# Kernel optimization log

Measured on AMD Instinct MI355X. Metric: run time of the kernel, lower is better.

## Reference

```python
import jax, jax.numpy as jnp
import numpy as np

N_NODES = 100000
N_EDGES = 1600000
IN_CH = 128
EMB = 64


def _init_linear(key, fan_in, fan_out):
    kw, kb = jax.random.split(key)
    scale = 1.0 / np.sqrt(fan_in)
    W = jax.random.uniform(kw, (fan_in, fan_out), jnp.float32, -scale, scale)
    b = jax.random.uniform(kb, (fan_out,), jnp.float32, -scale, scale)
    return W, b


def setup_inputs() -> dict:
    key = jax.random.key(0)
    ks = jax.random.split(key, 6)
    x = jax.random.normal(ks[0], (N_NODES, IN_CH), jnp.float32)
    edge_index = jax.random.randint(ks[1], (2, N_EDGES), 0, N_NODES)
    batch = jnp.zeros((N_NODES,), jnp.int32)
    # conv1 MLP: in_channels -> 32 -> 64 ; conv2 MLP: 64 -> 64 -> embedding_dim
    W1, b1 = _init_linear(ks[2], IN_CH, 32)
    W2, b2 = _init_linear(ks[3], 32, 64)
    W3, b3 = _init_linear(ks[4], 64, 64)
    W4, b4 = _init_linear(ks[5], 64, EMB)
    return {"x": x, "edge_index": edge_index, "batch": batch,
            "W1": W1, "b1": b1, "W2": W2, "b2": b2,
            "W3": W3, "b3": b3, "W4": W4, "b4": b4}


def _mlp(h, Wa, ba, Wb, bb):
    # PyG MLP: Linear -> act -> Linear (plain last layer)
    return jax.nn.relu(h @ Wa + ba) @ Wb + bb


def _gin_conv(x, src, dst, Wa, ba, Wb, bb):
    # out_i = MLP((1+eps)*x_i + sum_{j->i} x_j), eps = 0 (GINConv default)
    agg = jax.ops.segment_sum(x[src], dst, num_segments=N_NODES)  # [N, d]
    return _mlp(x + agg, Wa, ba, Wb, bb)


def reference(x, edge_index, batch, W1, b1, W2, b2, W3, b3, W4, b4):
    src, dst = edge_index[0], edge_index[1]
    h = jax.nn.relu(_gin_conv(x, src, dst, W1, b1, W2, b2))  # [N, 64]
    h = jax.nn.relu(_gin_conv(h, src, dst, W3, b3, W4, b4))  # [N, EMB]
    # batch is overwritten with zeros in the original forward -> single graph
    pooled = jnp.mean(h, axis=0, keepdims=True)  # [1, EMB]
    return h, pooled
```

## Files before the change

### kernel.cpp

```cpp
#include <hip/hip_runtime.h>

#define NN 100000
#define NE 1600000
#define NLB 256
#define CHUNK (NE / NLB)
#define NB 196
#define BN 512

__device__ __forceinline__ float bf2f(unsigned short u) {
    return __uint_as_float(((unsigned int)u) << 16);
}
__device__ __forceinline__ unsigned short f2bf(float f) {
    unsigned int u = __float_as_uint(f);
    return (unsigned short)((u + 0x7FFFu + ((u >> 16) & 1u)) >> 16);
}

__global__ __launch_bounds__(256) void k_front(const int* __restrict__ src,
                                               const int* __restrict__ dst,
                                               int* __restrict__ pairs,
                                               int* __restrict__ tstart,
                                               int* __restrict__ tcnt,
                                               int* __restrict__ btot,
                                               const float* __restrict__ x,
                                               const float* __restrict__ W1,
                                               unsigned short* __restrict__ z1) {
    __shared__ float Ws[128 * 32];
    __shared__ float xs[32][129];
    __shared__ int cnt[NB];
    __shared__ int sc[256];
    __shared__ int cur[NB];
    int tid = threadIdx.x;
    if (blockIdx.x < NLB) {
        int blk = blockIdx.x;
        int e0 = blk * CHUNK;
        for (int i = tid; i < NB; i += 256) cnt[i] = 0;
        __syncthreads();
        for (int i = tid; i < CHUNK; i += 256) atomicAdd(&cnt[dst[e0 + i] >> 9], 1);
        __syncthreads();
        sc[tid] = (tid < NB) ? cnt[tid] : 0;
        __syncthreads();
        for (int off = 1; off < 256; off <<= 1) {
            int v = (tid >= off) ? sc[tid - off] : 0;
            __syncthreads();
            sc[tid] += v;
            __syncthreads();
        }
        if (tid < NB) {
            int excl = sc[tid] - cnt[tid];
            cur[tid] = excl;
            tstart[blk * NB + tid] = excl;
            tcnt[blk * NB + tid]   = cnt[tid];
            atomicAdd(&btot[tid], cnt[tid]);
        }
        __syncthreads();
        for (int i = tid; i < CHUNK; i += 256) {
            int d = dst[e0 + i], s = src[e0 + i];
            int p = atomicAdd(&cur[d >> 9], 1);
            pairs[e0 + p] = ((d & (BN - 1)) << 17) | s;
        }
    } else {
        int bid = blockIdx.x - NLB;
        for (int i = tid; i < 1024; i += 256) {
            float4 w = ((const float4*)W1)[i];
            float* d = &Ws[i * 4];
            d[0] = w.x; d[1] = w.y; d[2] = w.z; d[3] = w.w;
        }
        int n_loc = tid >> 3;
        int j0    = (tid & 7) * 4;
        for (int base = bid * 32; base < NN; base += 1024 * 32) {
            __syncthreads();
            for (int t = tid; t < 1024; t += 256) {
                int n = t >> 5, c = t & 31;
                float4 v = ((const float4*)(x + (size_t)(base + n) * 128))[c];
                float* d = &xs[n][c * 4];
                d[0] = v.x; d[1] = v.y; d[2] = v.z; d[3] = v.w;
            }
            __syncthreads();
            float a0 = 0.f, a1 = 0.f, a2 = 0.f, a3 = 0.f;
            #pragma unroll 8
            for (int k = 0; k < 128; k++) {
                float xv = xs[n_loc][k];
                float4 w = *(const float4*)&Ws[k * 32 + j0];
                a0 = fmaf(xv, w.x, a0); a1 = fmaf(xv, w.y, a1);
                a2 = fmaf(xv, w.z, a2); a3 = fmaf(xv, w.w, a3);
            }
            ushort4 o = { f2bf(a0), f2bf(a1), f2bf(a2), f2bf(a3) };
            *(ushort4*)&z1[(size_t)(base + n_loc) * 32 + j0] = o;
        }
    }
}

__global__ __launch_bounds__(1024) void k_build(const int* __restrict__ pairs,
                                                const int* __restrict__ tstart,
                                                const int* __restrict__ tcnt,
                                                const int* __restrict__ btot,
                                                int* __restrict__ csr,
                                                int* __restrict__ row,
                                                int* __restrict__ rend) {
    __shared__ int segS[NLB], segL[NLB];
    __shared__ int ncnt[BN];
    __shared__ int nbase[BN + 1];
    __shared__ int sc[256];
    __shared__ int sc2[256];
    __shared__ int base_s;
    int tid = threadIdx.x, b = blockIdx.x;

    if (tid < 256) sc2[tid] = (tid < NB) ? btot[tid] : 0;
    __syncthreads();
    for (int off = 1; off < 256; off <<= 1) {
        int v = 0;
        if (tid < 256 && tid >= off) v = sc2[tid - off];
        __syncthreads();
        if (tid < 256) sc2[tid] += v;
        __syncthreads();
    }
    if (tid == 0) base_s = (b == 0) ? 0 : sc2[b - 1];
    if (tid < NLB) {
        segS[tid] = tid * CHUNK + tstart[tid * NB + b];
        segL[tid] = tcnt[tid * NB + b];
    }
    for (int i = tid; i < BN; i += 1024) ncnt[i] = 0;
    __syncthreads();

    int wave = tid >> 6, lane = tid & 63;
    for (int s = wave; s < NLB; s += 16) {
        int st = segS[s], len = segL[s];
        for (int i = lane; i < len; i += 64)
            atomicAdd(&ncnt[pairs[st + i] >> 17], 1);
    }
    __syncthreads();

    int c0 = 0, c1 = 0, tsum = 0;
    if (tid < 256) { c0 = ncnt[2 * tid]; c1 = ncnt[2 * tid + 1]; tsum = c0 + c1; sc[tid] = tsum; }
    __syncthreads();
    for (int off = 1; off < 256; off <<= 1) {
        int v = 0;
        if (tid < 256 && tid >= off) v = sc[tid - off];
        __syncthreads();
        if (tid < 256) sc[tid] += v;
        __syncthreads();
    }
    if (tid < 256) {
        int excl = sc[tid] - tsum;
        nbase[2 * tid]     = excl;
        nbase[2 * tid + 1] = excl + c0;
        if (tid == 255) nbase[BN] = sc[255];
    }
    __syncthreads();

    int base = base_s;
    if (tid < BN) {
        int n = b * BN + tid;
        if (n < NN) { row[n] = base + nbase[tid]; rend[n] = base + nbase[tid + 1]; }
        ncnt[tid] = 0;
    }
    __syncthreads();

    for (int s = wave; s < NLB; s += 16) {
        int st = segS[s], len = segL[s];
        for (int i = lane; i < len; i += 64) {
            int p = pairs[st + i];
            int ln = p >> 17;
            int pos = atomicAdd(&ncnt[ln], 1);
            csr[base + nbase[ln] + pos] = p & 0x1FFFF;
        }
    }
}

__global__ __launch_bounds__(256) void k_gather32(const int* __restrict__ row,
                                                  const int* __restrict__ rend,
                                                  const int* __restrict__ csr,
                                                  const unsigned short* __restrict__ z,
                                                  float* __restrict__ agg) {
    int n = blockIdx.x * 8 + (threadIdx.x >> 5);
    int f = threadIdx.x & 31;
    int j = row[n], e = rend[n];
    float a0 = 0.f, a1 = 0.f, a2 = 0.f, a3 = 0.f;
    for (; j + 3 < e; j += 4) {
        int i0 = csr[j], i1 = csr[j + 1], i2 = csr[j + 2], i3 = csr[j + 3];
        a0 += bf2f(z[(size_t)i0 * 32 + f]);
        a1 += bf2f(z[(size_t)i1 * 32 + f]);
        a2 += bf2f(z[(size_t)i2 * 32 + f]);
        a3 += bf2f(z[(size_t)i3 * 32 + f]);
    }
    for (; j < e; j++) a0 += bf2f(z[(size_t)csr[j] * 32 + f]);
    agg[(size_t)n * 32 + f] = (a0 + a1) + (a2 + a3);
}

__global__ __launch_bounds__(256) void k_gather64(const int* __restrict__ row,
                                                  const int* __restrict__ rend,
                                                  const int* __restrict__ csr,
                                                  const unsigned short* __restrict__ z,
                                                  float* __restrict__ agg) {
    int n = blockIdx.x * 4 + (threadIdx.x >> 6);
    int f = threadIdx.x & 63;
    int j = row[n], e = rend[n];
    float a0 = 0.f, a1 = 0.f, a2 = 0.f, a3 = 0.f;
    for (; j + 7 < e; j += 8) {
        int i0 = csr[j],     i1 = csr[j + 1], i2 = csr[j + 2], i3 = csr[j + 3];
        int i4 = csr[j + 4], i5 = csr[j + 5], i6 = csr[j + 6], i7 = csr[j + 7];
        float v0 = bf2f(z[(size_t)i0 * 64 + f]);
        float v1 = bf2f(z[(size_t)i1 * 64 + f]);
        float v2 = bf2f(z[(size_t)i2 * 64 + f]);
        float v3 = bf2f(z[(size_t)i3 * 64 + f]);
        float v4 = bf2f(z[(size_t)i4 * 64 + f]);
        float v5 = bf2f(z[(size_t)i5 * 64 + f]);
        float v6 = bf2f(z[(size_t)i6 * 64 + f]);
        float v7 = bf2f(z[(size_t)i7 * 64 + f]);
        a0 += v0 + v4; a1 += v1 + v5; a2 += v2 + v6; a3 += v3 + v7;
    }
    for (; j + 3 < e; j += 4) {
        int i0 = csr[j], i1 = csr[j + 1], i2 = csr[j + 2], i3 = csr[j + 3];
        a0 += bf2f(z[(size_t)i0 * 64 + f]);
        a1 += bf2f(z[(size_t)i1 * 64 + f]);
        a2 += bf2f(z[(size_t)i2 * 64 + f]);
        a3 += bf2f(z[(size_t)i3 * 64 + f]);
    }
    for (; j < e; j++) a0 += bf2f(z[(size_t)csr[j] * 64 + f]);
    agg[(size_t)n * 64 + f] = (a0 + a1) + (a2 + a3);
}

__global__ __launch_bounds__(256) void k_mid(const unsigned short* __restrict__ z1,
                                             const float* __restrict__ agg1,
                                             const float* __restrict__ b1,
                                             const float* __restrict__ W2,
                                             const float* __restrict__ b2,
                                             const float* __restrict__ W3,
                                             unsigned short* __restrict__ z2) {
    __shared__ float W2s[32 * 64];
    __shared__ float W3s[64 * 64];
    __shared__ float ts[32][33];
    __shared__ float hs[32 * 68];
    __shared__ float b1s[32], b2s[64];
    for (int i = threadIdx.x; i < 512; i += 256) {
        float4 w = ((const float4*)W2)[i];
        float* d = &W2s[i * 4];
        d[0] = w.x; d[1] = w.y; d[2] = w.z; d[3] = w.w;
    }
    for (int i = threadIdx.x; i < 1024; i += 256) {
        float4 w = ((const float4*)W3)[i];
        float* d = &W3s[i * 4];
        d[0] = w.x; d[1] = w.y; d[2] = w.z; d[3] = w.w;
    }
    if (threadIdx.x < 32) b1s[threadIdx.x] = b1[threadIdx.x];
    if (threadIdx.x >= 64 && threadIdx.x < 128) b2s[threadIdx.x - 64] = b2[threadIdx.x - 64];
    int n2 = threadIdx.x >> 4;
    int j0 = (threadIdx.x & 15) * 4;
    int na = 2 * n2, nb = 2 * n2 + 1;
    for (int base = blockIdx.x * 32; base < NN; base += gridDim.x * 32) {
        __syncthreads();
        #pragma unroll
        for (int r = 0; r < 4; r++) {
            int idx = threadIdx.x + 256 * r;
            int n = idx >> 5, f = idx & 31;
            ts[n][f] = fmaxf(bf2f(z1[(size_t)base * 32 + idx]) + agg1[(size_t)base * 32 + idx] + b1s[f], 0.f);
        }
        __syncthreads();
        {
            float a00=0,a01=0,a02=0,a03=0,a10=0,a11=0,a12=0,a13=0;
            #pragma unroll 8
            for (int k = 0; k < 32; k++) {
                float t0 = ts[na][k], t1 = ts[nb][k];
                float4 w = *(const float4*)&W2s[k * 64 + j0];
                a00=fmaf(t0,w.x,a00); a01=fmaf(t0,w.y,a01); a02=fmaf(t0,w.z,a02); a03=fmaf(t0,w.w,a03);
                a10=fmaf(t1,w.x,a10); a11=fmaf(t1,w.y,a11); a12=fmaf(t1,w.z,a12); a13=fmaf(t1,w.w,a13);
            }
            *(float4*)&hs[na * 68 + j0] = make_float4(fmaxf(a00+b2s[j0],0.f), fmaxf(a01+b2s[j0+1],0.f),
                                                      fmaxf(a02+b2s[j0+2],0.f), fmaxf(a03+b2s[j0+3],0.f));
            *(float4*)&hs[nb * 68 + j0] = make_float4(fmaxf(a10+b2s[j0],0.f), fmaxf(a11+b2s[j0+1],0.f),
                                                      fmaxf(a12+b2s[j0+2],0.f), fmaxf(a13+b2s[j0+3],0.f));
        }
        __syncthreads();
        {
            float a00=0,a01=0,a02=0,a03=0,a10=0,a11=0,a12=0,a13=0;
            #pragma unroll 8
            for (int k = 0; k < 64; k++) {
                float h0 = hs[na * 68 + k], h1 = hs[nb * 68 + k];
                float4 w = *(const float4*)&W3s[k * 64 + j0];
                a00=fmaf(h0,w.x,a00); a01=fmaf(h0,w.y,a01); a02=fmaf(h0,w.z,a02); a03=fmaf(h0,w.w,a03);
                a10=fmaf(h1,w.x,a10); a11=fmaf(h1,w.y,a11); a12=fmaf(h1,w.z,a12); a13=fmaf(h1,w.w,a13);
            }
            ushort4 oa = { f2bf(a00), f2bf(a01), f2bf(a02), f2bf(a03) };
            ushort4 ob = { f2bf(a10), f2bf(a11), f2bf(a12), f2bf(a13) };
            *(ushort4*)&z2[(size_t)(base + na) * 64 + j0] = oa;
            *(ushort4*)&z2[(size_t)(base + nb) * 64 + j0] = ob;
        }
    }
}

__global__ __launch_bounds__(256) void k_final(const unsigned short* __restrict__ z2,
                                               const float* __restrict__ agg2,
                                               const float* __restrict__ b3,
                                               const float* __restrict__ W4,
                                               const float* __restrict__ b4,
                                               float* __restrict__ out,
                                               float* __restrict__ gpool) {
    __shared__ float W4s[64 * 64];
    __shared__ float us[32 * 68];
    __shared__ float b3s[64], b4s[64], pool[64];
    for (int i = threadIdx.x; i < 1024; i += 256) {
        float4 w = ((const float4*)W4)[i];
        float* d = &W4s[i * 4];
        d[0] = w.x; d[1] = w.y; d[2] = w.z; d[3] = w.w;
    }
    if (threadIdx.x < 64) { b3s[threadIdx.x] = b3[threadIdx.x]; pool[threadIdx.x] = 0.f; }
    if (threadIdx.x >= 64 && threadIdx.x < 128) b4s[threadIdx.x - 64] = b4[threadIdx.x - 64];
    int n2 = threadIdx.x >> 4;
    int j0 = (threadIdx.x & 15) * 4;
    int na = 2 * n2, nb = 2 * n2 + 1;
    float p0 = 0.f, p1 = 0.f, p2 = 0.f, p3 = 0.f;
    for (int base = blockIdx.x * 32; base < NN; base += gridDim.x * 32) {
        __syncthreads();
        #pragma unroll
        for (int r = 0; r < 8; r++) {
            int idx = threadIdx.x + 256 * r;
            int n = idx >> 6, f = idx & 63;
            us[n * 68 + f] = fmaxf(bf2f(z2[(size_t)base * 64 + idx]) + agg2[(size_t)base * 64 + idx] + b3s[f], 0.f);
        }
        __syncthreads();
        float a00=0,a01=0,a02=0,a03=0,a10=0,a11=0,a12=0,a13=0;
        #pragma unroll 8
        for (int k = 0; k < 64; k++) {
            float u0 = us[na * 68 + k], u1 = us[nb * 68 + k];
            float4 w = *(const float4*)&W4s[k * 64 + j0];
            a00=fmaf(u0,w.x,a00); a01=fmaf(u0,w.y,a01); a02=fmaf(u0,w.z,a02); a03=fmaf(u0,w.w,a03);
            a10=fmaf(u1,w.x,a10); a11=fmaf(u1,w.y,a11); a12=fmaf(u1,w.z,a12); a13=fmaf(u1,w.w,a13);
        }
        float v00=fmaxf(a00+b4s[j0],0.f), v01=fmaxf(a01+b4s[j0+1],0.f);
        float v02=fmaxf(a02+b4s[j0+2],0.f), v03=fmaxf(a03+b4s[j0+3],0.f);
        float v10=fmaxf(a10+b4s[j0],0.f), v11=fmaxf(a11+b4s[j0+1],0.f);
        float v12=fmaxf(a12+b4s[j0+2],0.f), v13=fmaxf(a13+b4s[j0+3],0.f);
        *(float4*)&out[(size_t)(base + na) * 64 + j0] = make_float4(v00, v01, v02, v03);
        *(float4*)&out[(size_t)(base + nb) * 64 + j0] = make_float4(v10, v11, v12, v13);
        p0 += v00 + v10; p1 += v01 + v11; p2 += v02 + v12; p3 += v03 + v13;
    }
    __syncthreads();
    atomicAdd(&pool[j0 + 0], p0);
    atomicAdd(&pool[j0 + 1], p1);
    atomicAdd(&pool[j0 + 2], p2);
    atomicAdd(&pool[j0 + 3], p3);
    __syncthreads();
    if (threadIdx.x < 64) unsafeAtomicAdd(&gpool[threadIdx.x], pool[threadIdx.x]);
}

__global__ void k_pool(const float* __restrict__ gpool, float* __restrict__ out) {
    int t = threadIdx.x;
    if (t < 64) out[(size_t)NN * 64 + t] = gpool[t] * (1.0f / NN);
}

extern "C" void kernel_launch(void* const* d_in, const int* in_sizes, int n_in,
                              void* d_out, int out_size, void* d_ws, size_t ws_size,
                              hipStream_t stream) {
    const float* x  = (const float*)d_in[0];
    const int*   ei = (const int*)d_in[1];
    const float* W1 = (const float*)d_in[3];
    const float* b1 = (const float*)d_in[4];
    const float* W2 = (const float*)d_in[5];
    const float* b2 = (const float*)d_in[6];
    const float* W3 = (const float*)d_in[7];
    const float* b3 = (const float*)d_in[8];
    const float* W4 = (const float*)d_in[9];
    const float* b4 = (const float*)d_in[10];
    float* out = (float*)d_out;

    int*   ip     = (int*)d_ws;
    int*   tstart = ip;
    int*   tcnt   = ip + NLB * NB;
    int*   btot   = ip + 2 * NLB * NB;
    float* gpool  = (float*)(ip + 2 * NLB * NB + 196);
    int*   row    = ip + 2 * NLB * NB + 260;
    int*   rend   = row + NN;
    int*   csr    = rend + NN;
    int*   pairs  = csr + NE;
    unsigned short* z1b = (unsigned short*)(pairs + NE);
    float* agg1   = (float*)(pairs + NE + NN * 16);
    float* agg2   = (float*)pairs;
    unsigned short* z2b = (unsigned short*)(agg1 + (size_t)NN * 32);
    const int* src = ei;
    const int* dst = ei + NE;

    hipMemsetAsync(btot, 0, (196 + 64) * sizeof(int), stream);
    k_front<<<NLB + 1024, 256, 0, stream>>>(src, dst, pairs, tstart, tcnt, btot, x, W1, z1b);
    k_build<<<NB, 1024, 0, stream>>>(pairs, tstart, tcnt, btot, csr, row, rend);
    k_gather32<<<NN / 8, 256, 0, stream>>>(row, rend, csr, z1b, agg1);
    k_mid<<<1024, 256, 0, stream>>>(z1b, agg1, b1, W2, b2, W3, z2b);
    k_gather64<<<NN / 4, 256, 0, stream>>>(row, rend, csr, z2b, agg2);
    k_final<<<1024, 256, 0, stream>>>(z2b, agg2, b3, W4, b4, out, gpool);
    k_pool<<<1, 64, 0, stream>>>(gpool, out);
}
```

Before: 326.7 us.

## Fuse neighbor gathers into MLP kernels, removing fp32 agg buffers

Moves the CSR neighbor-sum gather for each layer into the MLP kernels, so each block gathers 32 nodes into shared memory and then runs the dense layers. This drops two kernel launches and the write and re-read of the fp32 aggregation buffers (agg1, agg2). In exchange, each block now reloads the weights for only 32 nodes (NN/32 blocks instead of a persistent grid of 1024), and gather latency is no longer hidden by a separate high-occupancy kernel.

Result: slower. 395.6 us (+21.1%).

```diff
diff --git a/kernel.cpp b/kernel.cpp
--- a/kernel.cpp
+++ b/kernel.cpp
@@ -167,61 +167,10 @@
     }
 }
 
-__global__ __launch_bounds__(256) void k_gather32(const int* __restrict__ row,
-                                                  const int* __restrict__ rend,
-                                                  const int* __restrict__ csr,
-                                                  const unsigned short* __restrict__ z,
-                                                  float* __restrict__ agg) {
-    int n = blockIdx.x * 8 + (threadIdx.x >> 5);
-    int f = threadIdx.x & 31;
-    int j = row[n], e = rend[n];
-    float a0 = 0.f, a1 = 0.f, a2 = 0.f, a3 = 0.f;
-    for (; j + 3 < e; j += 4) {
-        int i0 = csr[j], i1 = csr[j + 1], i2 = csr[j + 2], i3 = csr[j + 3];
-        a0 += bf2f(z[(size_t)i0 * 32 + f]);
-        a1 += bf2f(z[(size_t)i1 * 32 + f]);
-        a2 += bf2f(z[(size_t)i2 * 32 + f]);
-        a3 += bf2f(z[(size_t)i3 * 32 + f]);
-    }
-    for (; j < e; j++) a0 += bf2f(z[(size_t)csr[j] * 32 + f]);
-    agg[(size_t)n * 32 + f] = (a0 + a1) + (a2 + a3);
-}
-
-__global__ __launch_bounds__(256) void k_gather64(const int* __restrict__ row,
-                                                  const int* __restrict__ rend,
-                                                  const int* __restrict__ csr,
-                                                  const unsigned short* __restrict__ z,
-                                                  float* __restrict__ agg) {
-    int n = blockIdx.x * 4 + (threadIdx.x >> 6);
-    int f = threadIdx.x & 63;
-    int j = row[n], e = rend[n];
-    float a0 = 0.f, a1 = 0.f, a2 = 0.f, a3 = 0.f;
-    for (; j + 7 < e; j += 8) {
-        int i0 = csr[j],     i1 = csr[j + 1], i2 = csr[j + 2], i3 = csr[j + 3];
-        int i4 = csr[j + 4], i5 = csr[j + 5], i6 = csr[j + 6], i7 = csr[j + 7];
-        float v0 = bf2f(z[(size_t)i0 * 64 + f]);
-        float v1 = bf2f(z[(size_t)i1 * 64 + f]);
-        float v2 = bf2f(z[(size_t)i2 * 64 + f]);
-        float v3 = bf2f(z[(size_t)i3 * 64 + f]);
-        float v4 = bf2f(z[(size_t)i4 * 64 + f]);
-        float v5 = bf2f(z[(size_t)i5 * 64 + f]);
-        float v6 = bf2f(z[(size_t)i6 * 64 + f]);
-        float v7 = bf2f(z[(size_t)i7 * 64 + f]);
-        a0 += v0 + v4; a1 += v1 + v5; a2 += v2 + v6; a3 += v3 + v7;
-    }
-    for (; j + 3 < e; j += 4) {
-        int i0 = csr[j], i1 = csr[j + 1], i2 = csr[j + 2], i3 = csr[j + 3];
-        a0 += bf2f(z[(size_t)i0 * 64 + f]);
-        a1 += bf2f(z[(size_t)i1 * 64 + f]);
-        a2 += bf2f(z[(size_t)i2 * 64 + f]);
-        a3 += bf2f(z[(size_t)i3 * 64 + f]);
-    }
-    for (; j < e; j++) a0 += bf2f(z[(size_t)csr[j] * 64 + f]);
-    agg[(size_t)n * 64 + f] = (a0 + a1) + (a2 + a3);
-}
-
 __global__ __launch_bounds__(256) void k_mid(const unsigned short* __restrict__ z1,
-                                             const float* __restrict__ agg1,
+                                             const int* __restrict__ row,
+                                             const int* __restrict__ rend,
+                                             const int* __restrict__ csr,
                                              const float* __restrict__ b1,
                                              const float* __restrict__ W2,
                                              const float* __restrict__ b2,
@@ -232,64 +181,80 @@
     __shared__ float ts[32][33];
     __shared__ float hs[32 * 68];
     __shared__ float b1s[32], b2s[64];
-    for (int i = threadIdx.x; i < 512; i += 256) {
+    int tid = threadIdx.x;
+    for (int i = tid; i < 512; i += 256) {
         float4 w = ((const float4*)W2)[i];
         float* d = &W2s[i * 4];
         d[0] = w.x; d[1] = w.y; d[2] = w.z; d[3] = w.w;
     }
-    for (int i = threadIdx.x; i < 1024; i += 256) {
+    for (int i = tid; i < 1024; i += 256) {
         float4 w = ((const float4*)W3)[i];
         float* d = &W3s[i * 4];
         d[0] = w.x; d[1] = w.y; d[2] = w.z; d[3] = w.w;
     }
-    if (threadIdx.x < 32) b1s[threadIdx.x] = b1[threadIdx.x];
-    if (threadIdx.x >= 64 && threadIdx.x < 128) b2s[threadIdx.x - 64] = b2[threadIdx.x - 64];
-    int n2 = threadIdx.x >> 4;
-    int j0 = (threadIdx.x & 15) * 4;
+    if (tid < 32) b1s[tid] = b1[tid];
+    if (tid >= 64 && tid < 128) b2s[tid - 64] = b2[tid - 64];
+    __syncthreads();
+
+    int base = blockIdx.x * 32;
+    {
+        int hw = tid >> 5, f = tid & 31;
+        for (int r = 0; r < 4; r++) {
+            int ln = hw * 4 + r;
+            int n = base + ln;
+            int j = row[n], e = rend[n];
+            float a0 = bf2f(z1[(size_t)n * 32 + f]);
+            float a1 = 0.f, a2 = 0.f, a3 = 0.f;
+            for (; j + 3 < e; j += 4) {
+                int i0 = csr[j], i1 = csr[j + 1], i2 = csr[j + 2], i3 = csr[j + 3];
+                a0 += bf2f(z1[(size_t)i0 * 32 + f]);
+                a1 += bf2f(z1[(size_t)i1 * 32 + f]);
+                a2 += bf2f(z1[(size_t)i2 * 32 + f]);
+                a3 += bf2f(z1[(size_t)i3 * 32 + f]);
+            }
+            for (; j < e; j++) a0 += bf2f(z1[(size_t)csr[j] * 32 + f]);
+            ts[ln][f] = fmaxf(((a0 + a1) + (a2 + a3)) + b1s[f], 0.f);
+        }
+    }
+    __syncthreads();
+    int n2 = tid >> 4;
+    int j0 = (tid & 15) * 4;
     int na = 2 * n2, nb = 2 * n2 + 1;
-    for (int base = blockIdx.x * 32; base < NN; base += gridDim.x * 32) {
-        __syncthreads();
-        #pragma unroll
-        for (int r = 0; r < 4; r++) {
-            int idx = threadIdx.x + 256 * r;
-            int n = idx >> 5, f = idx & 31;
-            ts[n][f] = fmaxf(bf2f(z1[(size_t)base * 32 + idx]) + agg1[(size_t)base * 32 + idx] + b1s[f], 0.f);
-        }
-        __syncthreads();
-        {
-            float a00=0,a01=0,a02=0,a03=0,a10=0,a11=0,a12=0,a13=0;
-            #pragma unroll 8
-            for (int k = 0; k < 32; k++) {
-                float t0 = ts[na][k], t1 = ts[nb][k];
-                float4 w = *(const float4*)&W2s[k * 64 + j0];
-                a00=fmaf(t0,w.x,a00); a01=fmaf(t0,w.y,a01); a02=fmaf(t0,w.z,a02); a03=fmaf(t0,w.w,a03);
-                a10=fmaf(t1,w.x,a10); a11=fmaf(t1,w.y,a11); a12=fmaf(t1,w.z,a12); a13=fmaf(t1,w.w,a13);
-            }
-            *(float4*)&hs[na * 68 + j0] = make_float4(fmaxf(a00+b2s[j0],0.f), fmaxf(a01+b2s[j0+1],0.f),
-                                                      fmaxf(a02+b2s[j0+2],0.f), fmaxf(a03+b2s[j0+3],0.f));
-            *(float4*)&hs[nb * 68 + j0] = make_float4(fmaxf(a10+b2s[j0],0.f), fmaxf(a11+b2s[j0+1],0.f),
-                                                      fmaxf(a12+b2s[j0+2],0.f), fmaxf(a13+b2s[j0+3],0.f));
-        }
-        __syncthreads();
-        {
-            float a00=0,a01=0,a02=0,a03=0,a10=0,a11=0,a12=0,a13=0;
-            #pragma unroll 8
-            for (int k = 0; k < 64; k++) {
-                float h0 = hs[na * 68 + k], h1 = hs[nb * 68 + k];
-                float4 w = *(const float4*)&W3s[k * 64 + j0];
-                a00=fmaf(h0,w.x,a00); a01=fmaf(h0,w.y,a01); a02=fmaf(h0,w.z,a02); a03=fmaf(h0,w.w,a03);
-                a10=fmaf(h1,w.x,a10); a11=fmaf(h1,w.y,a11); a12=fmaf(h1,w.z,a12); a13=fmaf(h1,w.w,a13);
-            }
-            ushort4 oa = { f2bf(a00), f2bf(a01), f2bf(a02), f2bf(a03) };
-            ushort4 ob = { f2bf(a10), f2bf(a11), f2bf(a12), f2bf(a13) };
-            *(ushort4*)&z2[(size_t)(base + na) * 64 + j0] = oa;
-            *(ushort4*)&z2[(size_t)(base + nb) * 64 + j0] = ob;
-        }
+    {
+        float a00=0,a01=0,a02=0,a03=0,a10=0,a11=0,a12=0,a13=0;
+        #pragma unroll 8
+        for (int k = 0; k < 32; k++) {
+            float t0 = ts[na][k], t1 = ts[nb][k];
+            float4 w = *(const float4*)&W2s[k * 64 + j0];
+            a00=fmaf(t0,w.x,a00); a01=fmaf(t0,w.y,a01); a02=fmaf(t0,w.z,a02); a03=fmaf(t0,w.w,a03);
+            a10=fmaf(t1,w.x,a10); a11=fmaf(t1,w.y,a11); a12=fmaf(t1,w.z,a12); a13=fmaf(t1,w.w,a13);
+        }
+        *(float4*)&hs[na * 68 + j0] = make_float4(fmaxf(a00+b2s[j0],0.f), fmaxf(a01+b2s[j0+1],0.f),
+                                                  fmaxf(a02+b2s[j0+2],0.f), fmaxf(a03+b2s[j0+3],0.f));
+        *(float4*)&hs[nb * 68 + j0] = make_float4(fmaxf(a10+b2s[j0],0.f), fmaxf(a11+b2s[j0+1],0.f),
+                                                  fmaxf(a12+b2s[j0+2],0.f), fmaxf(a13+b2s[j0+3],0.f));
+    }
+    __syncthreads();
+    {
+        float a00=0,a01=0,a02=0,a03=0,a10=0,a11=0,a12=0,a13=0;
+        #pragma unroll 8
+        for (int k = 0; k < 64; k++) {
+            float h0 = hs[na * 68 + k], h1 = hs[nb * 68 + k];
+            float4 w = *(const float4*)&W3s[k * 64 + j0];
+            a00=fmaf(h0,w.x,a00); a01=fmaf(h0,w.y,a01); a02=fmaf(h0,w.z,a02); a03=fmaf(h0,w.w,a03);
+            a10=fmaf(h1,w.x,a10); a11=fmaf(h1,w.y,a11); a12=fmaf(h1,w.z,a12); a13=fmaf(h1,w.w,a13);
+        }
+        ushort4 oa = { f2bf(a00), f2bf(a01), f2bf(a02), f2bf(a03) };
+        ushort4 ob = { f2bf(a10), f2bf(a11), f2bf(a12), f2bf(a13) };
+        *(ushort4*)&z2[(size_t)(base + na) * 64 + j0] = oa;
+        *(ushort4*)&z2[(size_t)(base + nb) * 64 + j0] = ob;
     }
 }
 
 __global__ __launch_bounds__(256) void k_final(const unsigned short* __restrict__ z2,
-                                               const float* __restrict__ agg2,
+                                               const int* __restrict__ row,
+                                               const int* __restrict__ rend,
+                                               const int* __restrict__ csr,
                                                const float* __restrict__ b3,
                                                const float* __restrict__ W4,
                                                const float* __restrict__ b4,
@@ -298,49 +263,74 @@
     __shared__ float W4s[64 * 64];
     __shared__ float us[32 * 68];
     __shared__ float b3s[64], b4s[64], pool[64];
-    for (int i = threadIdx.x; i < 1024; i += 256) {
+    int tid = threadIdx.x;
+    for (int i = tid; i < 1024; i += 256) {
         float4 w = ((const float4*)W4)[i];
         float* d = &W4s[i * 4];
         d[0] = w.x; d[1] = w.y; d[2] = w.z; d[3] = w.w;
     }
-    if (threadIdx.x < 64) { b3s[threadIdx.x] = b3[threadIdx.x]; pool[threadIdx.x] = 0.f; }
-    if (threadIdx.x >= 64 && threadIdx.x < 128) b4s[threadIdx.x - 64] = b4[threadIdx.x - 64];
-    int n2 = threadIdx.x >> 4;
-    int j0 = (threadIdx.x & 15) * 4;
+    if (tid < 64) { b3s[tid] = b3[tid]; pool[tid] = 0.f; }
+    if (tid >= 64 && tid < 128) b4s[tid - 64] = b4[tid - 64];
+    __syncthreads();
+
+    int base = blockIdx.x * 32;
+    {
+        int w = tid >> 6, f = tid & 63;
+        for (int r = 0; r < 8; r++) {
+            int ln = w * 8 + r;
+            int n = base + ln;
+            int j = row[n], e = rend[n];
+            float a0 = bf2f(z2[(size_t)n * 64 + f]);
+            float a1 = 0.f, a2 = 0.f, a3 = 0.f;
+            for (; j + 7 < e; j += 8) {
+                int i0 = csr[j],     i1 = csr[j + 1], i2 = csr[j + 2], i3 = csr[j + 3];
+                int i4 = csr[j + 4], i5 = csr[j + 5], i6 = csr[j + 6], i7 = csr[j + 7];
+                float v0 = bf2f(z2[(size_t)i0 * 64 + f]);
+                float v1 = bf2f(z2[(size_t)i1 * 64 + f]);
+                float v2 = bf2f(z2[(size_t)i2 * 64 + f]);
+                float v3 = bf2f(z2[(size_t)i3 * 64 + f]);
+                float v4 = bf2f(z2[(size_t)i4 * 64 + f]);
+                float v5 = bf2f(z2[(size_t)i5 * 64 + f]);
+                float v6 = bf2f(z2[(size_t)i6 * 64 + f]);
+                float v7 = bf2f(z2[(size_t)i7 * 64 + f]);
+                a0 += v0 + v4; a1 += v1 + v5; a2 += v2 + v6; a3 += v3 + v7;
+            }
+            for (; j + 3 < e; j += 4) {
+                int i0 = csr[j], i1 = csr[j + 1], i2 = csr[j + 2], i3 = csr[j + 3];
+                a0 += bf2f(z2[(size_t)i0 * 64 + f]);
+                a1 += bf2f(z2[(size_t)i1 * 64 + f]);
+                a2 += bf2f(z2[(size_t)i2 * 64 + f]);
+                a3 += bf2f(z2[(size_t)i3 * 64 + f]);
+            }
+            for (; j < e; j++) a0 += bf2f(z2[(size_t)csr[j] * 64 + f]);
+            us[ln * 68 + f] = fmaxf(((a0 + a1) + (a2 + a3)) + b3s[f], 0.f);
+        }
+    }
+    __syncthreads();
+    int n2 = tid >> 4;
+    int j0 = (tid & 15) * 4;
     int na = 2 * n2, nb = 2 * n2 + 1;
-    float p0 = 0.f, p1 = 0.f, p2 = 0.f, p3 = 0.f;
-    for (int base = blockIdx.x * 32; base < NN; base += gridDim.x * 32) {
-        __syncthreads();
-        #pragma unroll
-        for (int r = 0; r < 8; r++) {
-            int idx = threadIdx.x + 256 * r;
-            int n = idx >> 6, f = idx & 63;
-            us[n * 68 + f] = fmaxf(bf2f(z2[(size_t)base * 64 + idx]) + agg2[(size_t)base * 64 + idx] + b3s[f], 0.f);
-        }
-        __syncthreads();
-        float a00=0,a01=0,a02=0,a03=0,a10=0,a11=0,a12=0,a13=0;
-        #pragma unroll 8
-        for (int k = 0; k < 64; k++) {
-            float u0 = us[na * 68 + k], u1 = us[nb * 68 + k];
-            float4 w = *(const float4*)&W4s[k * 64 + j0];
-            a00=fmaf(u0,w.x,a00); a01=fmaf(u0,w.y,a01); a02=fmaf(u0,w.z,a02); a03=fmaf(u0,w.w,a03);
-            a10=fmaf(u1,w.x,a10); a11=fmaf(u1,w.y,a11); a12=fmaf(u1,w.z,a12); a13=fmaf(u1,w.w,a13);
-        }
-        float v00=fmaxf(a00+b4s[j0],0.f), v01=fmaxf(a01+b4s[j0+1],0.f);
-        float v02=fmaxf(a02+b4s[j0+2],0.f), v03=fmaxf(a03+b4s[j0+3],0.f);
-        float v10=fmaxf(a10+b4s[j0],0.f), v11=fmaxf(a11+b4s[j0+1],0.f);
-        float v12=fmaxf(a12+b4s[j0+2],0.f), v13=fmaxf(a13+b4s[j0+3],0.f);
-        *(float4*)&out[(size_t)(base + na) * 64 + j0] = make_float4(v00, v01, v02, v03);
-        *(float4*)&out[(size_t)(base + nb) * 64 + j0] = make_float4(v10, v11, v12, v13);
-        p0 += v00 + v10; p1 += v01 + v11; p2 += v02 + v12; p3 += v03 + v13;
-    }
-    __syncthreads();
-    atomicAdd(&pool[j0 + 0], p0);
-    atomicAdd(&pool[j0 + 1], p1);
-    atomicAdd(&pool[j0 + 2], p2);
-    atomicAdd(&pool[j0 + 3], p3);
-    __syncthreads();
-    if (threadIdx.x < 64) unsafeAtomicAdd(&gpool[threadIdx.x], pool[threadIdx.x]);
+    float a00=0,a01=0,a02=0,a03=0,a10=0,a11=0,a12=0,a13=0;
+    #pragma unroll 8
+    for (int k = 0; k < 64; k++) {
+        float u0 = us[na * 68 + k], u1 = us[nb * 68 + k];
+        float4 w = *(const float4*)&W4s[k * 64 + j0];
+        a00=fmaf(u0,w.x,a00); a01=fmaf(u0,w.y,a01); a02=fmaf(u0,w.z,a02); a03=fmaf(u0,w.w,a03);
+        a10=fmaf(u1,w.x,a10); a11=fmaf(u1,w.y,a11); a12=fmaf(u1,w.z,a12); a13=fmaf(u1,w.w,a13);
+    }
+    float v00=fmaxf(a00+b4s[j0],0.f), v01=fmaxf(a01+b4s[j0+1],0.f);
+    float v02=fmaxf(a02+b4s[j0+2],0.f), v03=fmaxf(a03+b4s[j0+3],0.f);
+    float v10=fmaxf(a10+b4s[j0],0.f), v11=fmaxf(a11+b4s[j0+1],0.f);
+    float v12=fmaxf(a12+b4s[j0+2],0.f), v13=fmaxf(a13+b4s[j0+3],0.f);
+    *(float4*)&out[(size_t)(base + na) * 64 + j0] = make_float4(v00, v01, v02, v03);
+    *(float4*)&out[(size_t)(base + nb) * 64 + j0] = make_float4(v10, v11, v12, v13);
+    __syncthreads();
+    atomicAdd(&pool[j0 + 0], v00 + v10);
+    atomicAdd(&pool[j0 + 1], v01 + v11);
+    atomicAdd(&pool[j0 + 2], v02 + v12);
+    atomicAdd(&pool[j0 + 3], v03 + v13);
+    __syncthreads();
+    if (tid < 64) unsafeAtomicAdd(&gpool[tid], pool[tid]);
 }
 
 __global__ void k_pool(const float* __restrict__ gpool, float* __restrict__ out) {
@@ -373,18 +363,14 @@
     int*   csr    = rend + NN;
     int*   pairs  = csr + NE;
     unsigned short* z1b = (unsigned short*)(pairs + NE);
-    float* agg1   = (float*)(pairs + NE + NN * 16);
-    float* agg2   = (float*)pairs;
-    unsigned short* z2b = (unsigned short*)(agg1 + (size_t)NN * 32);
+    unsigned short* z2b = (unsigned short*)(pairs + NE + NN * 16);
     const int* src = ei;
     const int* dst = ei + NE;
 
     hipMemsetAsync(btot, 0, (196 + 64) * sizeof(int), stream);
     k_front<<<NLB + 1024, 256, 0, stream>>>(src, dst, pairs, tstart, tcnt, btot, x, W1, z1b);
     k_build<<<NB, 1024, 0, stream>>>(pairs, tstart, tcnt, btot, csr, row, rend);
-    k_gather32<<<NN / 8, 256, 0, stream>>>(row, rend, csr, z1b, agg1);
-    k_mid<<<1024, 256, 0, stream>>>(z1b, agg1, b1, W2, b2, W3, z2b);
-    k_gather64<<<NN / 4, 256, 0, stream>>>(row, rend, csr, z2b, agg2);
-    k_final<<<1024, 256, 0, stream>>>(z2b, agg2, b3, W4, b4, out, gpool);
+    k_mid<<<NN / 32, 256, 0, stream>>>(z1b, row, rend, csr, b1, W2, b2, W3, z2b);
+    k_final<<<NN / 32, 256, 0, stream>>>(z2b, row, rend, csr, b3, W4, b4, out, gpool);
     k_pool<<<1, 64, 0, stream>>>(gpool, out);
 }
```
